# Optimization experiments

Hardware: AMD Instinct MI355X
Metric: run time of the kernel (lower is better)

Reference implementation:

```python
import jax, jax.numpy as jnp
import numpy as np

# Faithful JAX port of the approxmatch EMD kernel (Fan et al.) wrapped by emdDist.
# 10 soft-assignment (auction-style) iterations with annealed temperature level=-4^j,
# j = 7..-1, final iteration level = 0. match is accumulated transport mass;
# cost[b] = sum_{k,l} match[b,k,l] * ||x1_k - x2_l||.

_EPS = 1e-9


def _approxmatch(xyz1, xyz2):
    # xyz1: (b, n, 3), xyz2: (b, m, 3)
    b, n, _ = xyz1.shape
    m = xyz2.shape[1]
    factorl = max(n, m) / n
    factorr = max(n, m) / m
    remainL = jnp.full((b, n), factorl, dtype=xyz1.dtype)   # mass left on xyz1 points
    remainR = jnp.full((b, m), factorr, dtype=xyz1.dtype)   # capacity left on xyz2 points
    # pairwise squared distances (b, n, m)
    d2 = jnp.sum((xyz1[:, :, None, :] - xyz2[:, None, :, :]) ** 2, axis=-1)
    match = jnp.zeros((b, n, m), dtype=xyz1.dtype)
    for j in range(7, -3, -1):  # j = 7, 6, ..., -1, -2
        level = 0.0 if j == -2 else -(4.0 ** j)
        # proposal weights from each left point, scaled by remaining right capacity
        w = jnp.exp(level * d2) * remainR[:, None, :]                      # (b,n,m)
        w = w / (jnp.sum(w, axis=-1, keepdims=True) + _EPS) * remainL[:, :, None]
        # right points accept at most their remaining capacity
        sumr = jnp.sum(w, axis=1) + _EPS                                   # (b,m)
        ratio = jnp.minimum(remainR / sumr, 1.0)                           # (b,m)
        delta = w * ratio[:, None, :]                                      # accepted transfer
        match = match + delta
        remainL = jnp.maximum(remainL - jnp.sum(delta, axis=-1), 0.0)
        remainR = jnp.maximum(remainR - jnp.sum(delta, axis=1), 0.0)
    return match, d2


def setup_inputs() -> dict:
    key = jax.random.key(0)
    k1, k2 = jax.random.split(key)
    B, N, M = 8, 4096, 4096
    input1 = jax.random.normal(k1, (B, N, 3), dtype=jnp.float32)
    input2 = jax.random.normal(k2, (B, M, 3), dtype=jnp.float32)
    return {"input1": input1, "input2": input2}


def reference(input1, input2):
    match, d2 = _approxmatch(input1, input2)
    # original CUDA backward treats match as a constant -> stop_gradient
    match = jax.lax.stop_gradient(match)
    dist = jnp.sqrt(jnp.maximum(d2, 1e-12))
    cost = jnp.sum(match * dist, axis=(1, 2))  # (b,)
    return cost
```

## Files before the change

kernel.cpp:

```cpp
#include <hip/hip_runtime.h>

#define NPTS 4096
#define NB   8
#define TPB  256
#define TPBR 128
#define MBLK 4
#define EPSC 1e-9f

#define EXP2(x)  __builtin_amdgcn_exp2f(x)
#define RCPF(x)  __builtin_amdgcn_rcpf(x)
#define SQRTF(x) __builtin_amdgcn_sqrtf(x)

__global__ __launch_bounds__(TPB) void sort_kernel(
    const float* __restrict__ x1, const float* __restrict__ x2,
    float4* __restrict__ x1p, float4* __restrict__ x2p,
    float4* __restrict__ bb)
{
  __shared__ unsigned int   hist[4096];
  __shared__ unsigned short codes[4096];
  __shared__ unsigned int   part[TPB];

  const int set = blockIdx.x, b = blockIdx.y;
  const float* src = set ? x2 : x1;
  float4* dst = set ? x2p : x1p;
  const int tid = threadIdx.x;

  for (int i = tid; i < 4096; i += TPB) hist[i] = 0;
  __syncthreads();

  for (int j = 0; j < NPTS / TPB; ++j) {
    int n = j * TPB + tid;
    const float* p = src + ((size_t)b * NPTS + n) * 3;
    int qx = min(max((int)((p[0] + 4.f) * 2.f), 0), 15);
    int qy = min(max((int)((p[1] + 4.f) * 2.f), 0), 15);
    int qz = min(max((int)((p[2] + 4.f) * 2.f), 0), 15);
    auto ex = [](int v) {
      return (v & 1) | ((v & 2) << 2) | ((v & 4) << 4) | ((v & 8) << 6);
    };
    int code = ex(qx) | (ex(qy) << 1) | (ex(qz) << 2);
    codes[n] = (unsigned short)code;
    atomicAdd(&hist[code], 1u);
  }
  __syncthreads();

  unsigned int loc[16], s = 0;
#pragma unroll
  for (int j = 0; j < 16; ++j) { loc[j] = s; s += hist[tid * 16 + j]; }
  part[tid] = s;
  __syncthreads();
  if (tid == 0) {
    unsigned int run = 0;
    for (int t = 0; t < TPB; ++t) { unsigned int v = part[t]; part[t] = run; run += v; }
  }
  __syncthreads();
  {
    unsigned int base = part[tid];
#pragma unroll
    for (int j = 0; j < 16; ++j) hist[tid * 16 + j] = base + loc[j];
  }
  __syncthreads();

  for (int j = 0; j < NPTS / TPB; ++j) {
    int n = j * TPB + tid;
    const float* p = src + ((size_t)b * NPTS + n) * 3;
    unsigned int pos = atomicAdd(&hist[codes[n]], 1u);
    dst[(size_t)b * NPTS + pos] = make_float4(p[0], p[1], p[2], 0.f);
  }
  __syncthreads();

  if (tid < 64) {
    float mnx = 1e30f, mny = 1e30f, mnz = 1e30f;
    float mxx = -1e30f, mxy = -1e30f, mxz = -1e30f;
    for (int j = 0; j < 64; ++j) {
      float4 p = dst[(size_t)b * NPTS + tid * 64 + j];
      mnx = fminf(mnx, p.x); mxx = fmaxf(mxx, p.x);
      mny = fminf(mny, p.y); mxy = fmaxf(mxy, p.y);
      mnz = fminf(mnz, p.z); mxz = fmaxf(mxz, p.z);
    }
    size_t bi = ((size_t)(set * NB + b) * 64 + tid) * 2;
    bb[bi + 0] = make_float4(mnx, mny, mnz, 0.f);
    bb[bi + 1] = make_float4(mxx, mxy, mxz, 0.f);
  }
}

__device__ __forceinline__ bool wave_cull(
    const float px[MBLK], const float py[MBLK], const float pz[MBLK],
    const float4* bbg, size_t gi, float sc)
{
  float mnx = fminf(fminf(px[0], px[1]), fminf(px[2], px[3]));
  float mny = fminf(fminf(py[0], py[1]), fminf(py[2], py[3]));
  float mnz = fminf(fminf(pz[0], pz[1]), fminf(pz[2], pz[3]));
  float mxx = fmaxf(fmaxf(px[0], px[1]), fmaxf(px[2], px[3]));
  float mxy = fmaxf(fmaxf(py[0], py[1]), fmaxf(py[2], py[3]));
  float mxz = fmaxf(fmaxf(pz[0], pz[1]), fmaxf(pz[2], pz[3]));
#pragma unroll
  for (int off = 1; off < 64; off <<= 1) {
    mnx = fminf(mnx, __shfl_xor(mnx, off));
    mny = fminf(mny, __shfl_xor(mny, off));
    mnz = fminf(mnz, __shfl_xor(mnz, off));
    mxx = fmaxf(mxx, __shfl_xor(mxx, off));
    mxy = fmaxf(mxy, __shfl_xor(mxy, off));
    mxz = fmaxf(mxz, __shfl_xor(mxz, off));
  }
  float4 smin = bbg[gi * 2 + 0], smax = bbg[gi * 2 + 1];
  float gx = fmaxf(0.f, fmaxf(sc * smin.x - mxx, mnx - sc * smax.x));
  float gy = fmaxf(0.f, fmaxf(sc * smin.y - mxy, mny - sc * smax.y));
  float gz = fmaxf(0.f, fmaxf(sc * smin.z - mxz, mnz - sc * smax.z));
  return fmaf(gx, gx, fmaf(gy, gy, gz * gz)) >= 126.f;
}

template<int MODE, bool CULL, bool PSKIP, int CHUNK>
__global__ __launch_bounds__(TPB) void ca_kernel(
    const float4* __restrict__ x2p, const float4* __restrict__ x1p,
    const float2* __restrict__ urbuf,
    float* __restrict__ dbufP, float* __restrict__ rsumP,
    const float4* __restrict__ bb2, float* __restrict__ out, float sc)
{
  __shared__ float4 x2s[CHUNK];
  __shared__ float2 urs[CHUNK];

  const int tid = threadIdx.x;
  const int nchunk = blockIdx.x, mseg = blockIdx.y, b = blockIdx.z;

  if (MODE == 0 && nchunk == 0 && mseg == 0 && tid == 0) out[b] = 0.f;

  for (int mm = tid; mm < CHUNK; mm += TPB) {
    int m = mseg * CHUNK + mm;
    float4 q = x2p[(size_t)b * NPTS + m];
    float sx = sc * q.x, sy = sc * q.y, sz = sc * q.z;
    float nq = fmaf(sz, sz, fmaf(sy, sy, sx * sx));
    x2s[mm] = make_float4(-2.f * sx, -2.f * sy, -2.f * sz, nq);
    urs[mm] = (MODE == 0) ? make_float2(0.f, 1.f) : urbuf[(size_t)b * NPTS + m];
  }
  __syncthreads();

  const int n0 = nchunk * (TPB * MBLK) + tid * MBLK;
  float px[MBLK], py[MBLK], pz[MBLK], np[MBLK], dacc[MBLK], racc[MBLK];
#pragma unroll
  for (int k = 0; k < MBLK; ++k) {
    float4 p = x1p[(size_t)b * NPTS + n0 + k];
    px[k] = sc * p.x; py[k] = sc * p.y; pz[k] = sc * p.z;
    np[k] = fmaf(pz[k], pz[k], fmaf(py[k], py[k], px[k] * px[k]));
    dacc[k] = 0.f; racc[k] = 0.f;
  }

  size_t base = ((size_t)mseg * NB + b) * NPTS + n0;
  if (CULL) {
    if (wave_cull(px, py, pz, bb2 + (size_t)b * 128, mseg, sc)) {
      *(float4*)&dbufP[base] = make_float4(0.f, 0.f, 0.f, 0.f);
      if (MODE >= 1) *(float4*)&rsumP[base] = make_float4(0.f, 0.f, 0.f, 0.f);
      return;
    }
  }

#pragma unroll 4
  for (int mm = 0; mm < CHUNK; ++mm) {
    float4 q = x2s[mm];
    float2 ur = urs[mm];
    float ds2[MBLK];
#pragma unroll
    for (int k = 0; k < MBLK; ++k)
      ds2[k] = fmaf(q.x, px[k], fmaf(q.y, py[k], fmaf(q.z, pz[k], np[k] + q.w)));
    if (MODE == 2) {
#pragma unroll
      for (int k = 0; k < MBLK; ++k) {
        dacc[k] += ur.y;
        racc[k] = fmaf(EXP2(-ds2[k]), ur.x, racc[k]);
      }
    } else {
      bool go = true;
      if (PSKIP) {
        float dmin = fminf(fminf(ds2[0], ds2[1]), fminf(ds2[2], ds2[3]));
        go = dmin < 126.f;
      }
      if (go) {
#pragma unroll
        for (int k = 0; k < MBLK; ++k) {
          float en = EXP2(-ds2[k]);
          dacc[k] = fmaf(en, ur.y, dacc[k]);
          if (MODE == 1) { float e2 = en * en; racc[k] = fmaf(e2 * e2, ur.x, racc[k]); }
        }
      }
    }
  }

  *(float4*)&dbufP[base] = make_float4(dacc[0], dacc[1], dacc[2], dacc[3]);
  if (MODE >= 1)
    *(float4*)&rsumP[base] = make_float4(racc[0], racc[1], racc[2], racc[3]);
}

template<int LVL0, bool CULL, bool PSKIP, int CHUNK>
__global__ __launch_bounds__(TPB) void b_kernel(
    const float4* __restrict__ x1p, const float* __restrict__ abuf,
    const float4* __restrict__ x2p,
    float* __restrict__ s0P, float* __restrict__ s1P,
    const float4* __restrict__ bb1, float sc, float inv_s)
{
  __shared__ float4 x1s[CHUNK];
  __shared__ float  as_[CHUNK];

  const int tid = threadIdx.x;
  const int mchunk = blockIdx.x, nsegi = blockIdx.y, b = blockIdx.z;

  for (int nn = tid; nn < CHUNK; nn += TPB) {
    int n = nsegi * CHUNK + nn;
    float4 p = x1p[(size_t)b * NPTS + n];
    float sx = sc * p.x, sy = sc * p.y, sz = sc * p.z;
    float npv = fmaf(sz, sz, fmaf(sy, sy, sx * sx));
    x1s[nn] = make_float4(-2.f * sx, -2.f * sy, -2.f * sz, npv);
    as_[nn] = abuf[(size_t)b * NPTS + n];
  }
  __syncthreads();

  const int m0 = mchunk * (TPB * MBLK) + tid * MBLK;
  float qx[MBLK], qy[MBLK], qz[MBLK], nq[MBLK], s0a[MBLK], s1a[MBLK];
#pragma unroll
  for (int k = 0; k < MBLK; ++k) {
    float4 q = x2p[(size_t)b * NPTS + m0 + k];
    qx[k] = sc * q.x; qy[k] = sc * q.y; qz[k] = sc * q.z;
    nq[k] = fmaf(qz[k], qz[k], fmaf(qy[k], qy[k], qx[k] * qx[k]));
    s0a[k] = 0.f; s1a[k] = 0.f;
  }

  size_t base = ((size_t)nsegi * NB + b) * NPTS + m0;
  if (CULL) {
    if (wave_cull(qx, qy, qz, bb1 + (size_t)b * 128, nsegi, sc)) {
      *(float4*)&s0P[base] = make_float4(0.f, 0.f, 0.f, 0.f);
      *(float4*)&s1P[base] = make_float4(0.f, 0.f, 0.f, 0.f);
      return;
    }
  }

#pragma unroll 4
  for (int nn = 0; nn < CHUNK; ++nn) {
    float4 p = x1s[nn];
    float av = as_[nn];
    float ds2[MBLK];
#pragma unroll
    for (int k = 0; k < MBLK; ++k)
      ds2[k] = fmaf(p.x, qx[k], fmaf(p.y, qy[k], fmaf(p.z, qz[k], nq[k] + p.w)));
    if (LVL0) {
#pragma unroll
      for (int k = 0; k < MBLK; ++k) {
        s0a[k] += av;
        s1a[k] = fmaf(av, SQRTF(__builtin_fabsf(ds2[k])), s1a[k]);
      }
    } else {
      bool go = true;
      if (PSKIP) {
        float dmin = fminf(fminf(ds2[0], ds2[1]), fminf(ds2[2], ds2[3]));
        go = dmin < 126.f;
      }
      if (go) {
#pragma unroll
        for (int k = 0; k < MBLK; ++k) {
          float tt = av * EXP2(-ds2[k]);
          s0a[k] += tt;
          s1a[k] = fmaf(tt, SQRTF(__builtin_fabsf(ds2[k])), s1a[k]);
        }
      }
    }
  }

  *(float4*)&s0P[base] = make_float4(s0a[0], s0a[1], s0a[2], s0a[3]);
  *(float4*)&s1P[base] = make_float4(s1a[0] * inv_s, s1a[1] * inv_s,
                                     s1a[2] * inv_s, s1a[3] * inv_s);
}

template<int NSEG>
__global__ __launch_bounds__(TPBR) void r1_kernel(
    const float* __restrict__ dbufP, const float* __restrict__ rsumP,
    float* __restrict__ lbuf, float* __restrict__ dtot,
    float* __restrict__ abuf, int iter)
{
  const int idx = blockIdx.x * TPBR + threadIdx.x;
  const int b = idx >> 12, n = idx & (NPTS - 1);
  const int off = b * NPTS + n;

  float dnew = 0.f;
#pragma unroll
  for (int s = 0; s < NSEG; ++s) dnew += dbufP[((size_t)s * NB + b) * NPTS + n];

  float rl;
  if (iter == 0) {
    rl = 1.f;
  } else {
    float rlp = lbuf[off];
    float ap  = rlp * RCPF(dtot[off] + EPSC);
    float rs = 0.f;
#pragma unroll
    for (int s = 0; s < NSEG; ++s) rs += rsumP[((size_t)s * NB + b) * NPTS + n];
    rl = fmaxf(rlp - ap * rs, 0.f);
  }
  lbuf[off] = rl;
  dtot[off] = dnew;
  abuf[off] = rl * RCPF(dnew + EPSC);
}

template<int NSEG, bool LAST>
__global__ __launch_bounds__(TPBR) void r2_kernel(
    const float* __restrict__ s0P, const float* __restrict__ s1P,
    float2* __restrict__ urbuf, float* __restrict__ out, int iter)
{
  __shared__ float red[TPBR];
  const int idx = blockIdx.x * TPBR + threadIdx.x;
  const int b = idx >> 12, m = idx & (NPTS - 1);
  const int off = b * NPTS + m;

  float s0 = 0.f, s1 = 0.f;
#pragma unroll
  for (int s = 0; s < NSEG; ++s) {
    s0 += s0P[((size_t)s * NB + b) * NPTS + m];
    s1 += s1P[((size_t)s * NB + b) * NPTS + m];
  }
  float rr    = (iter == 0) ? 1.f : urbuf[off].y;
  float sumr  = fmaf(rr, s0, EPSC);
  float ratio = fminf(rr * RCPF(sumr), 1.f);
  float u     = rr * ratio;
  if (!LAST) urbuf[off] = make_float2(u, fmaxf(rr - u * s0, 0.f));

  red[threadIdx.x] = u * s1;
  __syncthreads();
  for (int s = TPBR / 2; s > 0; s >>= 1) {
    if (threadIdx.x < s) red[threadIdx.x] += red[threadIdx.x + s];
    __syncthreads();
  }
  if (threadIdx.x == 0) atomicAdd(out + b, red[0]);
}

template<int NSEG>
static void run_all(const float* x1, const float* x2, float* out, float* ws,
                    hipStream_t stream)
{
  constexpr int CHUNK = NPTS / NSEG;
  const size_t plane = (size_t)NB * NPTS;

  float*  bufA = ws;
  float*  bufB = bufA + (size_t)NSEG * plane;
  float4* x1p  = (float4*)(bufB + (size_t)NSEG * plane);
  float4* x2p  = x1p + plane;
  float*  dtot = (float*)(x2p + plane);
  float*  lbuf = dtot + plane;
  float*  abuf = lbuf + plane;
  float2* urbuf = (float2*)(abuf + plane);
  float4* bb   = (float4*)(urbuf + plane);
  float4* bb1  = bb;
  float4* bb2  = bb + (size_t)NB * 128;

  const double L2E = 1.4426950408889634074;
  const double lv[10] = {-16384.0, -4096.0, -1024.0, -256.0, -64.0,
                         -16.0, -4.0, -1.0, -0.25, 0.0};
  float scl[10], inv_s[10];
  for (int i = 0; i < 10; ++i) {
    double c2 = lv[i] * L2E;
    scl[i]   = (i == 9) ? 1.f : (float)sqrt(-c2);
    inv_s[i] = (i == 9) ? 1.f : (float)(1.0 / sqrt(-c2));
  }

  dim3 gmain(NPTS / (TPB * MBLK), NSEG, NB), bmain(TPB);
  dim3 gr(NPTS * NB / TPBR), br(TPBR);

  sort_kernel<<<dim3(2, NB), bmain, 0, stream>>>(x1, x2, x1p, x2p, bb);

  ca_kernel<0, true, true, CHUNK><<<gmain, bmain, 0, stream>>>(
      x2p, x1p, urbuf, bufA, bufB, bb2, out, scl[0]);

  for (int i = 0; i < 10; ++i) {
    r1_kernel<NSEG><<<gr, br, 0, stream>>>(bufA, bufB, lbuf, dtot, abuf, i);

    if (i <= 4)
      b_kernel<0, true, true, CHUNK><<<gmain, bmain, 0, stream>>>(
          x1p, abuf, x2p, bufA, bufB, bb1, scl[i], inv_s[i]);
    else if (i == 5)
      b_kernel<0, true, false, CHUNK><<<gmain, bmain, 0, stream>>>(
          x1p, abuf, x2p, bufA, bufB, bb1, scl[i], inv_s[i]);
    else if (i <= 8)
      b_kernel<0, false, false, CHUNK><<<gmain, bmain, 0, stream>>>(
          x1p, abuf, x2p, bufA, bufB, bb1, scl[i], inv_s[i]);
    else
      b_kernel<1, false, false, CHUNK><<<gmain, bmain, 0, stream>>>(
          x1p, abuf, x2p, bufA, bufB, bb1, 1.f, 1.f);

    if (i < 9)
      r2_kernel<NSEG, false><<<gr, br, 0, stream>>>(bufA, bufB, urbuf, out, i);
    else
      r2_kernel<NSEG, true><<<gr, br, 0, stream>>>(bufA, bufB, urbuf, out, i);

    if (i <= 3)
      ca_kernel<1, true, true, CHUNK><<<gmain, bmain, 0, stream>>>(
          x2p, x1p, urbuf, bufA, bufB, bb2, out, scl[i + 1]);
    else if (i <= 5)
      ca_kernel<1, true, false, CHUNK><<<gmain, bmain, 0, stream>>>(
          x2p, x1p, urbuf, bufA, bufB, bb2, out, scl[i + 1]);
    else if (i <= 7)
      ca_kernel<1, false, false, CHUNK><<<gmain, bmain, 0, stream>>>(
          x2p, x1p, urbuf, bufA, bufB, bb2, out, scl[i + 1]);
    else if (i == 8)
      ca_kernel<2, false, false, CHUNK><<<gmain, bmain, 0, stream>>>(
          x2p, x1p, urbuf, bufA, bufB, bb2, out, scl[8]);
  }
}

extern "C" void kernel_launch(void* const* d_in, const int* in_sizes, int n_in,
                              void* d_out, int out_size, void* d_ws, size_t ws_size,
                              hipStream_t stream) {
  const float* x1 = (const float*)d_in[0];
  const float* x2 = (const float*)d_in[1];
  float* out = (float*)d_out;
  float* ws  = (float*)d_ws;

  const size_t plane = (size_t)NB * NPTS;
  auto need = [&](int nseg) {
    return (size_t)(2 * nseg + 13) * plane * sizeof(float)
         + (size_t)2048 * sizeof(float4);
  };

  if (ws_size >= need(64))      run_all<64>(x1, x2, out, ws, stream);
  else if (ws_size >= need(32)) run_all<32>(x1, x2, out, ws, stream);
  else                          run_all<16>(x1, x2, out, ws, stream);
}
```

Baseline: 1.010 ms.

## Split partial-sum reduction across warps in r1/r2 and extend pruned-path iterations

The r1 and r2 reduction kernels now give each output element eight thread slices, each summing NSEG/8 segment partials. The slices are combined through shared memory, replacing a single thread serially summing all NSEG partials. This raises memory-level parallelism for the segment reduction, at the cost of extra syncthreads and idle threads in the final step. Separately, the template selection for b_kernel and ca_kernel shifts one iteration later, so iteration 5 uses the more aggressive (pruned) variant. That may cut work but risks accuracy if pruning is too loose at that temperature.

```diff
diff --git a/kernel.cpp b/kernel.cpp
--- a/kernel.cpp
+++ b/kernel.cpp
@@ -3,7 +3,6 @@
 #define NPTS 4096
 #define NB   8
 #define TPB  256
-#define TPBR 128
 #define MBLK 4
 #define EPSC 1e-9f
 
@@ -268,64 +267,95 @@
 }
 
 template<int NSEG>
-__global__ __launch_bounds__(TPBR) void r1_kernel(
+__global__ __launch_bounds__(256) void r1_kernel(
     const float* __restrict__ dbufP, const float* __restrict__ rsumP,
     float* __restrict__ lbuf, float* __restrict__ dtot,
     float* __restrict__ abuf, int iter)
 {
-  const int idx = blockIdx.x * TPBR + threadIdx.x;
-  const int b = idx >> 12, n = idx & (NPTS - 1);
-  const int off = b * NPTS + n;
-
-  float dnew = 0.f;
-#pragma unroll
-  for (int s = 0; s < NSEG; ++s) dnew += dbufP[((size_t)s * NB + b) * NPTS + n];
-
-  float rl;
-  if (iter == 0) {
-    rl = 1.f;
-  } else {
-    float rlp = lbuf[off];
-    float ap  = rlp * RCPF(dtot[off] + EPSC);
-    float rs = 0.f;
-#pragma unroll
-    for (int s = 0; s < NSEG; ++s) rs += rsumP[((size_t)s * NB + b) * NPTS + n];
-    rl = fmaxf(rlp - ap * rs, 0.f);
-  }
-  lbuf[off] = rl;
-  dtot[off] = dnew;
-  abuf[off] = rl * RCPF(dnew + EPSC);
+  constexpr int SL = 8, EPB = 32, PPS = NSEG / SL;
+  __shared__ float redD[SL][EPB];
+  __shared__ float redR[SL][EPB];
+
+  const int e  = threadIdx.x & (EPB - 1);
+  const int sl = threadIdx.x / EPB;
+  const int idx = blockIdx.x * EPB + e;
+  const size_t plane = (size_t)NB * NPTS;
+
+  float ad = 0.f, ar = 0.f;
+#pragma unroll
+  for (int s = 0; s < PPS; ++s)
+    ad += dbufP[(size_t)(sl * PPS + s) * plane + idx];
+  if (iter > 0) {
+#pragma unroll
+    for (int s = 0; s < PPS; ++s)
+      ar += rsumP[(size_t)(sl * PPS + s) * plane + idx];
+  }
+  redD[sl][e] = ad;
+  redR[sl][e] = ar;
+  __syncthreads();
+
+  if (sl == 0) {
+    float dnew = 0.f, rs = 0.f;
+#pragma unroll
+    for (int s = 0; s < SL; ++s) { dnew += redD[s][e]; rs += redR[s][e]; }
+    float rl = 1.f;
+    if (iter > 0) {
+      float rlp = lbuf[idx];
+      float ap  = rlp * RCPF(dtot[idx] + EPSC);
+      rl = fmaxf(rlp - ap * rs, 0.f);
+    }
+    lbuf[idx] = rl;
+    dtot[idx] = dnew;
+    abuf[idx] = rl * RCPF(dnew + EPSC);
+  }
 }
 
 template<int NSEG, bool LAST>
-__global__ __launch_bounds__(TPBR) void r2_kernel(
+__global__ __launch_bounds__(256) void r2_kernel(
     const float* __restrict__ s0P, const float* __restrict__ s1P,
     float2* __restrict__ urbuf, float* __restrict__ out, int iter)
 {
-  __shared__ float red[TPBR];
-  const int idx = blockIdx.x * TPBR + threadIdx.x;
-  const int b = idx >> 12, m = idx & (NPTS - 1);
-  const int off = b * NPTS + m;
-
-  float s0 = 0.f, s1 = 0.f;
-#pragma unroll
-  for (int s = 0; s < NSEG; ++s) {
-    s0 += s0P[((size_t)s * NB + b) * NPTS + m];
-    s1 += s1P[((size_t)s * NB + b) * NPTS + m];
-  }
-  float rr    = (iter == 0) ? 1.f : urbuf[off].y;
-  float sumr  = fmaf(rr, s0, EPSC);
-  float ratio = fminf(rr * RCPF(sumr), 1.f);
-  float u     = rr * ratio;
-  if (!LAST) urbuf[off] = make_float2(u, fmaxf(rr - u * s0, 0.f));
-
-  red[threadIdx.x] = u * s1;
-  __syncthreads();
-  for (int s = TPBR / 2; s > 0; s >>= 1) {
-    if (threadIdx.x < s) red[threadIdx.x] += red[threadIdx.x + s];
-    __syncthreads();
-  }
-  if (threadIdx.x == 0) atomicAdd(out + b, red[0]);
+  constexpr int SL = 8, EPB = 32, PPS = NSEG / SL;
+  __shared__ float redA[SL][EPB];
+  __shared__ float redB[SL][EPB];
+
+  const int e  = threadIdx.x & (EPB - 1);
+  const int sl = threadIdx.x / EPB;
+  const int idx = blockIdx.x * EPB + e;
+  const int b = idx >> 12;
+  const size_t plane = (size_t)NB * NPTS;
+
+  float a0 = 0.f, a1 = 0.f;
+#pragma unroll
+  for (int s = 0; s < PPS; ++s) {
+    a0 += s0P[(size_t)(sl * PPS + s) * plane + idx];
+    a1 += s1P[(size_t)(sl * PPS + s) * plane + idx];
+  }
+  redA[sl][e] = a0;
+  redB[sl][e] = a1;
+  __syncthreads();
+
+  float cpart = 0.f;
+  if (sl == 0) {
+    float s0 = 0.f, s1 = 0.f;
+#pragma unroll
+    for (int s = 0; s < SL; ++s) { s0 += redA[s][e]; s1 += redB[s][e]; }
+    float rr    = (iter == 0) ? 1.f : urbuf[idx].y;
+    float sumr  = fmaf(rr, s0, EPSC);
+    float ratio = fminf(rr * RCPF(sumr), 1.f);
+    float u     = rr * ratio;
+    if (!LAST) urbuf[idx] = make_float2(u, fmaxf(rr - u * s0, 0.f));
+    cpart = u * s1;
+  }
+  __syncthreads();
+  if (sl == 0) redA[0][e] = cpart;
+  __syncthreads();
+  if (threadIdx.x == 0) {
+    float acc = 0.f;
+#pragma unroll
+    for (int j = 0; j < EPB; ++j) acc += redA[0][j];
+    atomicAdd(out + b, acc);
+  }
 }
 
 template<int NSEG>
@@ -358,7 +388,7 @@
   }
 
   dim3 gmain(NPTS / (TPB * MBLK), NSEG, NB), bmain(TPB);
-  dim3 gr(NPTS * NB / TPBR), br(TPBR);
+  dim3 gr(NB * NPTS / 32), br(256);
 
   sort_kernel<<<dim3(2, NB), bmain, 0, stream>>>(x1, x2, x1p, x2p, bb);
 
@@ -368,11 +398,8 @@
   for (int i = 0; i < 10; ++i) {
     r1_kernel<NSEG><<<gr, br, 0, stream>>>(bufA, bufB, lbuf, dtot, abuf, i);
 
-    if (i <= 4)
+    if (i <= 5)
       b_kernel<0, true, true, CHUNK><<<gmain, bmain, 0, stream>>>(
-          x1p, abuf, x2p, bufA, bufB, bb1, scl[i], inv_s[i]);
-    else if (i == 5)
-      b_kernel<0, true, false, CHUNK><<<gmain, bmain, 0, stream>>>(
           x1p, abuf, x2p, bufA, bufB, bb1, scl[i], inv_s[i]);
     else if (i <= 8)
       b_kernel<0, false, false, CHUNK><<<gmain, bmain, 0, stream>>>(
@@ -386,10 +413,10 @@
     else
       r2_kernel<NSEG, true><<<gr, br, 0, stream>>>(bufA, bufB, urbuf, out, i);
 
-    if (i <= 3)
+    if (i <= 4)
       ca_kernel<1, true, true, CHUNK><<<gmain, bmain, 0, stream>>>(
           x2p, x1p, urbuf, bufA, bufB, bb2, out, scl[i + 1]);
-    else if (i <= 5)
+    else if (i == 5)
       ca_kernel<1, true, false, CHUNK><<<gmain, bmain, 0, stream>>>(
           x2p, x1p, urbuf, bufA, bufB, bb2, out, scl[i + 1]);
     else if (i <= 7)
```

Result: faster. 987.7 us (-2.2%).
